# Performance work log

Hardware: AMD Instinct MI355X
Metric: run time of the kernel (lower is better)

## Reference

```python
import jax, jax.numpy as jnp
import numpy as np

N_C = 64
D = 128

def setup_inputs() -> dict:
    key = jax.random.key(0)
    embeddings = jax.random.normal(key, (1024, N_C * D), dtype=jnp.float32)
    return {"embeddings": embeddings}

def reference(embeddings) -> jnp.ndarray:
    two_b, _ = embeddings.shape
    B = two_b // 2
    # (2, B, n_c, d), softmax over last dim
    q = jax.nn.softmax(embeddings.reshape(2, B, N_C, D), axis=-1)
    q_a, q_b = q[0], q[1]  # (B, n_c, d)

    self_sim_loss = -(q_a * q_b).sum() / (B * N_C)

    q_a2 = q_a * q_a
    q_b2 = q_b * q_b
    # Faithful to the repeat/repeat_interleave + bmm: block (i, j) of the
    # (n_c^2, d, d) product equals q2[:, j].T @ q2[:, i]  -> einsum over batch.
    prod_a = jnp.einsum('bjc,bid->ijcd', q_a2, q_a2)  # (n_c, n_c, d, d)
    prod_b = jnp.einsum('bjc,bid->ijcd', q_b2, q_b2)

    # mask out diagonal cluster pairs i == j (done before sqrt in original;
    # entries are strictly positive so masking after sqrt is identical)
    offdiag = (~jnp.eye(N_C, dtype=bool))[:, :, None, None]  # (n_c, n_c, 1, 1)

    raw_a = jnp.where(offdiag, jnp.sqrt(prod_a), 0.0).sum()
    raw_b = jnp.where(offdiag, jnp.sqrt(prod_b), 0.0).sum()

    scale = (N_C * N_C - N_C) * (B ** 0.5)
    cluster_loss = -(raw_a / scale + raw_b / scale) / 2
    return self_sim_loss + cluster_loss
```

## Files before the change

kernel.cpp:

```cpp
#include <hip/hip_runtime.h>
#include <cstdint>
#include <cstddef>

#define NCLUS 64
#define DIM   128
#define BATCH 512
#define QCOLS 8192
#define NPAIR 2016
#define TSTRB (QCOLS * BATCH)
#define FP8SCALE 256.0f

typedef float f32x4 __attribute__((ext_vector_type(4)));
typedef long  lx2  __attribute__((ext_vector_type(2)));


__device__ __forceinline__ void ld_lds16(const void* g, void* l) {
  __builtin_amdgcn_global_load_lds(
      (__attribute__((address_space(1))) void*)g,
      (__attribute__((address_space(3))) void*)l, 16, 0, 0);
}

#define SYNC_VM4()  asm volatile("s_waitcnt vmcnt(4)\n\ts_barrier" ::: "memory")
#define SYNC_VM0()  asm volatile("s_waitcnt vmcnt(0)\n\ts_barrier" ::: "memory")
#define SYNC_LGKM() asm volatile("s_waitcnt lgkmcnt(0)\n\ts_barrier" ::: "memory")

__global__ __launch_bounds__(256) void softmax_q2_kernel(
    const float* __restrict__ emb, uint8_t* __restrict__ q2t,
    float* __restrict__ dotPart) {
  __shared__ unsigned short T[2][64][130];
  __shared__ float red[4];
  const int c   = blockIdx.y;
  const int bq8 = blockIdx.x;
  const int tid = threadIdx.x;
  const int w = tid >> 6, lane = tid & 63;
  const int bl = tid >> 2;
  const int qd = tid & 3;
  const int b = bq8 * 64 + bl;

  float qa[32];
  float dot = 0.f;
#pragma unroll
  for (int t = 0; t < 2; ++t) {
    const float4* rp = (const float4*)(emb + ((size_t)(t * BATCH + b) * QCOLS +
                                              (size_t)c * DIM + qd * 32));
    float f[32];
#pragma unroll
    for (int u = 0; u < 8; ++u) {
      float4 v = rp[u];
      f[4*u] = v.x; f[4*u+1] = v.y; f[4*u+2] = v.z; f[4*u+3] = v.w;
    }
    float mx = f[0];
#pragma unroll
    for (int j = 1; j < 32; ++j) mx = fmaxf(mx, f[j]);
    mx = fmaxf(mx, __shfl_xor(mx, 1));
    mx = fmaxf(mx, __shfl_xor(mx, 2));
    float s = 0.f;
#pragma unroll
    for (int j = 0; j < 32; ++j) { f[j] = __expf(f[j] - mx); s += f[j]; }
    s += __shfl_xor(s, 1);
    s += __shfl_xor(s, 2);
    float inv = 1.0f / s;
    uint32_t* Tu = (uint32_t*)&T[t][bl][qd * 32];
#pragma unroll
    for (int j = 0; j < 32; j += 2) {
      float q0 = f[j] * inv, q1 = f[j + 1] * inv;
      if (t == 0) { qa[j] = q0; qa[j + 1] = q1; }
      else        { dot += qa[j] * q0 + qa[j + 1] * q1; }
      int pk2 = __builtin_amdgcn_cvt_pk_fp8_f32(q0 * q0 * FP8SCALE,
                                                q1 * q1 * FP8SCALE, 0, false);
      Tu[j >> 1] = ((uint32_t)pk2 & 0xFFu) | (((uint32_t)pk2 & 0xFF00u) << 8);
    }
  }
  __syncthreads();

#pragma unroll
  for (int it = 0; it < 4; ++it) {
    int ch = it * 256 + tid;
    int t = ch >> 9, d = (ch >> 2) & 127, b16 = ch & 3;
    uint32_t w0 = 0, w1 = 0, w2 = 0, w3 = 0;
#pragma unroll
    for (int r = 0; r < 4; ++r) {
      w0 |= ((uint32_t)T[t][b16 * 8 + r][d] & 0xFFu) << (8 * r);
      w1 |= ((uint32_t)T[t][b16 * 8 + 4 + r][d] & 0xFFu) << (8 * r);
      w2 |= ((uint32_t)T[t][32 + b16 * 8 + r][d] & 0xFFu) << (8 * r);
      w3 |= ((uint32_t)T[t][32 + b16 * 8 + 4 + r][d] & 0xFFu) << (8 * r);
    }
    size_t off = (size_t)t * TSTRB + (size_t)(c * DIM + d) * BATCH +
                 (size_t)bq8 * 64 + b16 * 16;
    uint4 o; o.x = w0; o.y = w1; o.z = w2; o.w = w3;
    *(uint4*)(q2t + off) = o;
  }

#pragma unroll
  for (int off = 1; off < 64; off <<= 1) dot += __shfl_xor(dot, off);
  if (lane == 0) red[w] = dot;
  __syncthreads();
  if (tid == 0) dotPart[blockIdx.y * 8 + blockIdx.x] = red[0] + red[1] + red[2] + red[3];
}

__global__ __launch_bounds__(256, 4) void gram_sqrt_kernel(
    const uint8_t* __restrict__ q2t, float* __restrict__ Spart) {
  __shared__ uint8_t L[32768 + 16];

  int sidx = ((int)blockIdx.x & 7) * 252 + ((int)blockIdx.x >> 3);
  int q = sidx, gi = 0;
  while (q >= 64 * gi + 28) { q -= 64 * gi + 28; ++gi; }
  int I, J;
  if (q < 64 * gi) {
    int gj = q >> 6, r = q & 63;
    I = gi * 8 + (r >> 3);
    J = gj * 8 + (r & 7);
  } else {
    int dq = q - 64 * gi;
    int il = 1;
    while (il * (il + 1) / 2 <= dq) ++il;
    I = gi * 8 + il;
    J = gi * 8 + (dq - il * (il - 1) / 2);
  }

  const uint8_t* baseA = q2t + (size_t)J * (DIM * BATCH);
  const uint8_t* baseB = q2t + (size_t)I * (DIM * BATCH);

  const int tid  = threadIdx.x;
  const int lane = tid & 63, w = tid >> 6;
  const int wm = w & 1, wn = w >> 1;

  const int t0 = tid, t1 = 256 + tid;
  const int r0s = t0 >> 2, r1s = t1 >> 2;
  const int c0s = ((t0 & 3) - ((r0s >> 1) & 3)) & 3;
  const int c1s = ((t1 & 3) - ((r1s >> 1) & 3)) & 3;
  const size_t g0 = (size_t)r0s * BATCH + c0s * 16;
  const size_t g1 = (size_t)r1s * BATCH + c1s * 16;
  uint8_t* Lb = L;
  const int ldsw = w * 1024;

  const int l15 = lane & 15, qtr = lane >> 4;
  const int sig = ((qtr + (l15 >> 1)) & 3) * 16;
  const int ApO = wm * 4096 + l15 * 64 + sig;
  const int BpO = 8192 + wn * 4096 + l15 * 64 + sig;

  f32x4 acc[4][4];
#pragma unroll
  for (int i = 0; i < 4; ++i)
#pragma unroll
    for (int j = 0; j < 4; ++j) acc[i][j] = (f32x4){0.f, 0.f, 0.f, 0.f};

  float S0 = 0.f, S1 = 0.f;

  ld_lds16(baseA + g0, Lb + ldsw);
  ld_lds16(baseA + g1, Lb + 4096 + ldsw);
  ld_lds16(baseB + g0, Lb + 8192 + ldsw);
  ld_lds16(baseB + g1, Lb + 12288 + ldsw);

  for (int m = 0; m < 16; ++m) {
    if (m < 15) {
      const int mi = m + 1;
      const int bb = (mi & 1) << 14;
      const size_t ck = (size_t)(mi >> 3) * TSTRB + (size_t)(mi & 7) * 64;
      ld_lds16(baseA + ck + g0, Lb + bb + ldsw);
      ld_lds16(baseA + ck + g1, Lb + bb + 4096 + ldsw);
      ld_lds16(baseB + ck + g0, Lb + bb + 8192 + ldsw);
      ld_lds16(baseB + ck + g1, Lb + bb + 12288 + ldsw);
      SYNC_VM4();
    } else {
      SYNC_VM0();
    }

    const int be = (m & 1) << 14;
    lx2 a[4], b[4];
#pragma unroll
    for (int i = 0; i < 4; ++i) {
      a[i] = *(const lx2*)(Lb + be + ApO + i * 1024);
      b[i] = *(const lx2*)(Lb + be + BpO + i * 1024);
    }
#pragma unroll
    for (int i = 0; i < 4; ++i)
#pragma unroll
      for (int j = 0; j < 4; ++j)
        acc[i][j] = __builtin_amdgcn_mfma_f32_16x16x32_fp8_fp8(a[i].x, b[j].x, acc[i][j], 0, 0, 0);
#pragma unroll
    for (int i = 0; i < 4; ++i)
#pragma unroll
      for (int j = 0; j < 4; ++j)
        acc[i][j] = __builtin_amdgcn_mfma_f32_16x16x32_fp8_fp8(a[i].y, b[j].y, acc[i][j], 0, 0, 0);

    if (m == 7) {
#pragma unroll
      for (int i = 0; i < 4; ++i)
#pragma unroll
        for (int j = 0; j < 4; ++j) {
#pragma unroll
          for (int e = 0; e < 4; ++e) S0 += sqrtf(acc[i][j][e]);
          acc[i][j] = (f32x4){0.f, 0.f, 0.f, 0.f};
        }
    }

    SYNC_LGKM();
  }

#pragma unroll
  for (int i = 0; i < 4; ++i)
#pragma unroll
    for (int j = 0; j < 4; ++j)
#pragma unroll
      for (int e = 0; e < 4; ++e) S1 += sqrtf(acc[i][j][e]);

  float local = (S0 + S1) * (1.0f / 256.0f);
#pragma unroll
  for (int off = 1; off < 64; off <<= 1) local += __shfl_xor(local, off);
  float* fred = (float*)(L + 32768);
  if (lane == 0) fred[w] = local;
  __syncthreads();
  if (tid == 0) Spart[blockIdx.x] = fred[0] + fred[1] + fred[2] + fred[3];
}

__global__ __launch_bounds__(256) void finalize_kernel(
    const float* __restrict__ P, float* __restrict__ out) {
  __shared__ float rd[8];
  const int tid = threadIdx.x;
  float d = 0.f, s = 0.f;
  for (int i = tid; i < 512; i += 256) d += P[i];
  for (int i = tid; i < NPAIR; i += 256) s += P[512 + i];
#pragma unroll
  for (int off = 1; off < 64; off <<= 1) { d += __shfl_xor(d, off); s += __shfl_xor(s, off); }
  const int w = tid >> 6;
  if ((tid & 63) == 0) { rd[w] = d; rd[4 + w] = s; }
  __syncthreads();
  if (tid == 0) {
    float dt = rd[0] + rd[1] + rd[2] + rd[3];
    float st = rd[4] + rd[5] + rd[6] + rd[7];
    out[0] = -dt / 32768.0f - st / (4032.0f * 22.62741699796952f);
  }
}

extern "C" void kernel_launch(void* const* d_in, const int* in_sizes, int n_in,
                              void* d_out, int out_size, void* d_ws, size_t ws_size,
                              hipStream_t stream) {
  const float* emb = (const float*)d_in[0];
  float* out = (float*)d_out;
  float* P = (float*)d_ws;
  uint8_t* q2t = (uint8_t*)d_ws + 16384;

  softmax_q2_kernel<<<dim3(8, 64), 256, 0, stream>>>(emb, q2t, P);
  gram_sqrt_kernel<<<dim3(NPAIR), 256, 0, stream>>>(q2t, P + 512);
  finalize_kernel<<<1, 256, 0, stream>>>(P, out);
}
```

Before: 133.9 us.

## Triple-buffer gram LDS pipeline and fold finalize into last-block reduction

The gram kernel's LDS staging grows from two buffers to three. Loads are now issued two chunks ahead, and one barrier per iteration replaces the separate wait-and-barrier pairs, which cuts barrier stalls and exposed load latency. The separate finalize kernel is removed: an atomic counter lets the last finishing block do the final reduction, which saves one kernel launch but adds a memset. The larger LDS use lowers the occupancy bound from 4 to 3 blocks per CU.

```diff
diff --git a/kernel.cpp b/kernel.cpp
--- a/kernel.cpp
+++ b/kernel.cpp
@@ -20,9 +20,8 @@
       (__attribute__((address_space(3))) void*)l, 16, 0, 0);
 }
 
-#define SYNC_VM4()  asm volatile("s_waitcnt vmcnt(4)\n\ts_barrier" ::: "memory")
-#define SYNC_VM0()  asm volatile("s_waitcnt vmcnt(0)\n\ts_barrier" ::: "memory")
-#define SYNC_LGKM() asm volatile("s_waitcnt lgkmcnt(0)\n\ts_barrier" ::: "memory")
+#define SYNC_VM4L() asm volatile("s_waitcnt vmcnt(4) lgkmcnt(0)\n\ts_barrier" ::: "memory")
+#define SYNC_VM0L() asm volatile("s_waitcnt vmcnt(0) lgkmcnt(0)\n\ts_barrier" ::: "memory")
 
 __global__ __launch_bounds__(256) void softmax_q2_kernel(
     const float* __restrict__ emb, uint8_t* __restrict__ q2t,
@@ -98,9 +97,10 @@
   if (tid == 0) dotPart[blockIdx.y * 8 + blockIdx.x] = red[0] + red[1] + red[2] + red[3];
 }
 
-__global__ __launch_bounds__(256, 4) void gram_sqrt_kernel(
-    const uint8_t* __restrict__ q2t, float* __restrict__ Spart) {
-  __shared__ uint8_t L[32768 + 16];
+__global__ __launch_bounds__(256, 3) void gram_sqrt_kernel(
+    const uint8_t* __restrict__ q2t, float* __restrict__ P,
+    unsigned int* __restrict__ cnt, float* __restrict__ out) {
+  __shared__ uint8_t L[49152 + 16];
 
   int sidx = ((int)blockIdx.x & 7) * 252 + ((int)blockIdx.x >> 3);
   int q = sidx, gi = 0;
@@ -151,27 +151,33 @@
   ld_lds16(baseA + g1, Lb + 4096 + ldsw);
   ld_lds16(baseB + g0, Lb + 8192 + ldsw);
   ld_lds16(baseB + g1, Lb + 12288 + ldsw);
-
+  {
+    const size_t ck = 64;
+    ld_lds16(baseA + ck + g0, Lb + 16384 + ldsw);
+    ld_lds16(baseA + ck + g1, Lb + 16384 + 4096 + ldsw);
+    ld_lds16(baseB + ck + g0, Lb + 16384 + 8192 + ldsw);
+    ld_lds16(baseB + ck + g1, Lb + 16384 + 12288 + ldsw);
+  }
+
+  int beR = 0;
   for (int m = 0; m < 16; ++m) {
-    if (m < 15) {
-      const int mi = m + 1;
-      const int bb = (mi & 1) << 14;
+    if (m < 15) SYNC_VM4L(); else SYNC_VM0L();
+
+    if (m <= 13) {
+      const int mi = m + 2;
+      int bp = beR + 32768; if (bp >= 49152) bp -= 49152;
       const size_t ck = (size_t)(mi >> 3) * TSTRB + (size_t)(mi & 7) * 64;
-      ld_lds16(baseA + ck + g0, Lb + bb + ldsw);
-      ld_lds16(baseA + ck + g1, Lb + bb + 4096 + ldsw);
-      ld_lds16(baseB + ck + g0, Lb + bb + 8192 + ldsw);
-      ld_lds16(baseB + ck + g1, Lb + bb + 12288 + ldsw);
-      SYNC_VM4();
-    } else {
-      SYNC_VM0();
-    }
-
-    const int be = (m & 1) << 14;
+      ld_lds16(baseA + ck + g0, Lb + bp + ldsw);
+      ld_lds16(baseA + ck + g1, Lb + bp + 4096 + ldsw);
+      ld_lds16(baseB + ck + g0, Lb + bp + 8192 + ldsw);
+      ld_lds16(baseB + ck + g1, Lb + bp + 12288 + ldsw);
+    }
+
     lx2 a[4], b[4];
 #pragma unroll
     for (int i = 0; i < 4; ++i) {
-      a[i] = *(const lx2*)(Lb + be + ApO + i * 1024);
-      b[i] = *(const lx2*)(Lb + be + BpO + i * 1024);
+      a[i] = *(const lx2*)(Lb + beR + ApO + i * 1024);
+      b[i] = *(const lx2*)(Lb + beR + BpO + i * 1024);
     }
 #pragma unroll
     for (int i = 0; i < 4; ++i)
@@ -195,7 +201,7 @@
         }
     }
 
-    SYNC_LGKM();
+    beR += 16384; if (beR >= 49152) beR = 0;
   }
 
 #pragma unroll
@@ -208,28 +214,32 @@
   float local = (S0 + S1) * (1.0f / 256.0f);
 #pragma unroll
   for (int off = 1; off < 64; off <<= 1) local += __shfl_xor(local, off);
-  float* fred = (float*)(L + 32768);
+  float* fred = (float*)(L + 49152);
   if (lane == 0) fred[w] = local;
   __syncthreads();
-  if (tid == 0) Spart[blockIdx.x] = fred[0] + fred[1] + fred[2] + fred[3];
-}
-
-__global__ __launch_bounds__(256) void finalize_kernel(
-    const float* __restrict__ P, float* __restrict__ out) {
-  __shared__ float rd[8];
-  const int tid = threadIdx.x;
-  float d = 0.f, s = 0.f;
-  for (int i = tid; i < 512; i += 256) d += P[i];
-  for (int i = tid; i < NPAIR; i += 256) s += P[512 + i];
-#pragma unroll
-  for (int off = 1; off < 64; off <<= 1) { d += __shfl_xor(d, off); s += __shfl_xor(s, off); }
-  const int w = tid >> 6;
-  if ((tid & 63) == 0) { rd[w] = d; rd[4 + w] = s; }
-  __syncthreads();
+
+  __shared__ int lastFlag;
   if (tid == 0) {
-    float dt = rd[0] + rd[1] + rd[2] + rd[3];
-    float st = rd[4] + rd[5] + rd[6] + rd[7];
-    out[0] = -dt / 32768.0f - st / (4032.0f * 22.62741699796952f);
+    P[512 + blockIdx.x] = fred[0] + fred[1] + fred[2] + fred[3];
+    __threadfence();
+    lastFlag = (atomicAdd(cnt, 1u) == (unsigned)(NPAIR - 1));
+  }
+  __syncthreads();
+
+  if (lastFlag) {
+    __threadfence();
+    float d = 0.f, s = 0.f;
+    for (int i = tid; i < 512; i += 256) d += P[i];
+    for (int i = tid; i < NPAIR; i += 256) s += P[512 + i];
+#pragma unroll
+    for (int off = 1; off < 64; off <<= 1) { d += __shfl_xor(d, off); s += __shfl_xor(s, off); }
+    if (lane == 0) { fred[w] = d; fred[4 + w] = s; }
+    __syncthreads();
+    if (tid == 0) {
+      float dt = fred[0] + fred[1] + fred[2] + fred[3];
+      float st = fred[4] + fred[5] + fred[6] + fred[7];
+      out[0] = -dt / 32768.0f - st / (4032.0f * 22.62741699796952f);
+    }
   }
 }
 
@@ -238,10 +248,11 @@
                               hipStream_t stream) {
   const float* emb = (const float*)d_in[0];
   float* out = (float*)d_out;
-  float* P = (float*)d_ws;
+  unsigned int* cnt = (unsigned int*)d_ws;
+  float* P = (float*)((char*)d_ws + 64);
   uint8_t* q2t = (uint8_t*)d_ws + 16384;
 
+  hipMemsetAsync(d_ws, 0, 4, stream);
   softmax_q2_kernel<<<dim3(8, 64), 256, 0, stream>>>(emb, q2t, P);
-  gram_sqrt_kernel<<<dim3(NPAIR), 256, 0, stream>>>(q2t, P + 512);
-  finalize_kernel<<<1, 256, 0, stream>>>(P, out);
-}
+  gram_sqrt_kernel<<<dim3(NPAIR), 256, 0, stream>>>(q2t, P, cnt, out);
+}
```

New measurement: 176.1 us. +31.5%, slower.
